# Kernel optimization log

Measured on AMD Instinct MI355X. Metric: run time of the kernel, lower is better.

Reference implementation:

```python
import jax, jax.numpy as jnp
import numpy as np

D_MODEL = 1024
N_HEADS = 16
D_K = 64  # per-head dim and the scaling denominator used by the module
NEG = -1e9  # stand-in for -inf in masked_fill (rows are never fully masked)


def setup_inputs() -> dict:
    key = jax.random.key(0)
    ks = jax.random.split(key, 8)
    B, M, N = 2, 2048, 2048
    q = jax.random.normal(ks[0], (B, M, D_MODEL), dtype=jnp.float32)
    k = jax.random.normal(ks[1], (B, N, D_MODEL), dtype=jnp.float32)
    v = jax.random.normal(ks[2], (B, N, D_MODEL), dtype=jnp.float32)
    mask = jax.random.randint(ks[3], (B, M, N), 0, 2).astype(jnp.bool_)
    # xavier_uniform for square [d,d] weights: limit = sqrt(6/(d+d))
    lim = float(np.sqrt(6.0 / (D_MODEL + D_MODEL)))
    Wq = jax.random.uniform(ks[4], (D_MODEL, D_MODEL), jnp.float32, -lim, lim)
    Wk = jax.random.uniform(ks[5], (D_MODEL, D_MODEL), jnp.float32, -lim, lim)
    Wv = jax.random.uniform(ks[6], (D_MODEL, D_MODEL), jnp.float32, -lim, lim)
    Wo = jax.random.uniform(ks[7], (D_MODEL, D_MODEL), jnp.float32, -lim, lim)
    return {"q": q, "k": k, "v": v, "mask": mask,
            "Wq": Wq, "Wk": Wk, "Wv": Wv, "Wo": Wo}


def _split_heads(x):
    # (B, S, D) -> (B, H, S, Dh); the torch split/cat-on-batch trick is
    # mathematically identical to this standard head reshape.
    B, S, _ = x.shape
    return x.reshape(B, S, N_HEADS, D_K).transpose(0, 2, 1, 3)


def reference(q, k, v, mask, Wq, Wk, Wv, Wo):
    qw = _split_heads(q @ Wq.T)  # (B,H,M,Dh)
    kw = _split_heads(k @ Wk.T)  # (B,H,N,Dh)
    vw = _split_heads(v @ Wv.T)  # (B,H,N,Dh)
    scores = jnp.einsum('bhmd,bhnd->bhmn', qw, kw)
    scores = jnp.where(mask[:, None, :, :], NEG, scores)
    attn = jax.nn.softmax(scores / jnp.sqrt(jnp.float32(D_K)), axis=-1)
    ctx = jnp.einsum('bhmn,bhnd->bhmd', attn, vw)
    B, _, M, _ = ctx.shape
    ctx = ctx.transpose(0, 2, 1, 3).reshape(B, M, D_MODEL)
    return ctx @ Wo.T
```

## Files before the change

kernel.cpp:

```cpp
#include <hip/hip_runtime.h>
#include <hip/hip_bf16.h>
#include <stdint.h>
#include <string.h>

#define SEQ   2048
#define DM    1024
#define NH    16
#define NB    2

typedef __attribute__((ext_vector_type(8))) short bf16x8;
typedef __attribute__((ext_vector_type(4))) float f32x4;
typedef unsigned short u16;
typedef unsigned int   u32;

__device__ __forceinline__ u16 f2bf(float f) {
    u32 u = __float_as_uint(f);
    u += 0x7FFF + ((u >> 16) & 1);
    return (u16)(u >> 16);
}
__device__ __forceinline__ u32 pk2bf(float a, float b) {
    __hip_bfloat162 p = __float22bfloat162_rn(make_float2(a, b));
    u32 u; memcpy(&u, &p, 4); return u;
}
__device__ __forceinline__ float fexp2(float x) {
#if __has_builtin(__builtin_amdgcn_exp2f)
    return __builtin_amdgcn_exp2f(x);
#else
    return exp2f(x);
#endif
}
__device__ __forceinline__ void gl_lds16(const void* g, void* l) {
    __builtin_amdgcn_global_load_lds(
        (const __attribute__((address_space(1))) u32*)g,
        (__attribute__((address_space(3))) u32*)l, 16, 0, 0);
}
__device__ __forceinline__ void wbar_vm3() { asm volatile("s_waitcnt vmcnt(3)\ns_barrier" ::: "memory"); }
__device__ __forceinline__ void wbar_vm4() { asm volatile("s_waitcnt vmcnt(4)\ns_barrier" ::: "memory"); }
__device__ __forceinline__ void wbar_vm6() { asm volatile("s_waitcnt vmcnt(6)\ns_barrier" ::: "memory"); }
__device__ __forceinline__ void vm_drain() { asm volatile("s_waitcnt vmcnt(0)" ::: "memory"); }

struct CvtArgs {
    const float* s[7];
    u16* d[7];
    float scale[7];
    int start[8];
};
__global__ __launch_bounds__(256) void cvt_kernel(CvtArgs a) {
    int bid = blockIdx.x;
    int seg = 0;
#pragma unroll
    for (int i = 1; i < 7; ++i) if (bid >= a.start[i]) seg = i;
    float sc = a.scale[seg];
    size_t base = (size_t)(bid - a.start[seg]) * 2048 + threadIdx.x * 8;
    const float4* s4 = (const float4*)(a.s[seg] + base);
    float4 x = s4[0], y = s4[1];
    u32 r[4];
    r[0] = pk2bf(x.x*sc, x.y*sc); r[1] = pk2bf(x.z*sc, x.w*sc);
    r[2] = pk2bf(y.x*sc, y.y*sc); r[3] = pk2bf(y.z*sc, y.w*sc);
    *(uint4*)(a.d[seg] + base) = *(uint4*)r;
}

__global__ void maskpack_kernel(const int* __restrict__ mask,
                                unsigned int* __restrict__ bits) {
    int gid = blockIdx.x * 256 + threadIdx.x;
    int m = mask[gid];
    unsigned long long bal = __ballot(m != 0);
    int lane = threadIdx.x & 63;
    if (lane == 0)       bits[gid >> 5] = (u32)(bal & 0xFFFFFFFFull);
    else if (lane == 32) bits[gid >> 5] = (u32)(bal >> 32);
}

template<int RT>
__device__ __forceinline__ void gemm_body(const u16* __restrict__ A,
                                          const u16* __restrict__ Bm,
                                          void* __restrict__ Y,
                                          int rtile, int ctile, int mode,
                                          u16* sA, u16* sB) {
    constexpr int ABUF = RT * 32 * 32;
    constexpr int BBUF = 128 * 32;
    const int tid  = threadIdx.x;
    const int wv   = tid >> 6, lane = tid & 63;
    const int quad = lane >> 4, ln = lane & 15;
    const int wr   = wv >> 1,  wc  = wv & 1;

    const int lr4 = lane >> 2;
    const int lcc = ((lane & 3) ^ ((lane >> 3) & 3)) * 8;

    const u16* gA[RT/2]; u16* lA[RT/2];
#pragma unroll
    for (int s = 0; s < RT/2; ++s) {
        int seg = wv * (RT/2) + s;
        gA[s] = A + (size_t)(rtile * (RT*32) + seg*16 + lr4) * 1024 + lcc;
        lA[s] = sA + seg * 512;
    }
    const u16* gB[2]; u16* lB[2];
#pragma unroll
    for (int s = 0; s < 2; ++s) {
        int seg = wv * 2 + s;
        gB[s] = Bm + (size_t)(ctile * 128 + seg*16 + lr4) * 1024 + lcc;
        lB[s] = sB + seg * 512;
    }

    f32x4 acc[RT][4];
#pragma unroll
    for (int i = 0; i < RT; ++i)
#pragma unroll
        for (int j = 0; j < 4; ++j) acc[i][j] = (f32x4){0.f,0.f,0.f,0.f};

    const int c0 = (quad ^ ((ln >> 1) & 3)) * 8;

#pragma unroll
    for (int s = 0; s < RT/2; ++s) gl_lds16(gA[s], lA[s]);
#pragma unroll
    for (int s = 0; s < 2; ++s)    gl_lds16(gB[s], lB[s]);
#pragma unroll
    for (int s = 0; s < RT/2; ++s) gl_lds16(gA[s] + 32, lA[s] + ABUF);
#pragma unroll
    for (int s = 0; s < 2; ++s)    gl_lds16(gB[s] + 32, lB[s] + BBUF);

    int bc = 0, bp = 2;
    for (int kt = 0; kt < 32; ++kt) {
        if (RT == 4) wbar_vm4(); else wbar_vm3();
        int pk = (kt + 2) & 31;
#pragma unroll
        for (int s = 0; s < RT/2; ++s) gl_lds16(gA[s] + pk*32, lA[s] + bp*ABUF);
#pragma unroll
        for (int s = 0; s < 2; ++s)    gl_lds16(gB[s] + pk*32, lB[s] + bp*BBUF);

        const u16* sAb = sA + bc * ABUF;
        const u16* sBb = sB + bc * BBUF;
        bf16x8 af[RT], bfr[4];
#pragma unroll
        for (int rt = 0; rt < RT; ++rt)
            af[rt] = *(const bf16x8*)(sAb + (wr*(RT*16) + rt*16 + ln) * 32 + c0);
#pragma unroll
        for (int ct = 0; ct < 4; ++ct)
            bfr[ct] = *(const bf16x8*)(sBb + (wc*64 + ct*16 + ln) * 32 + c0);
#pragma unroll
        for (int rt = 0; rt < RT; ++rt)
#pragma unroll
            for (int ct = 0; ct < 4; ++ct)
                acc[rt][ct] = __builtin_amdgcn_mfma_f32_16x16x32_bf16(
                    af[rt], bfr[ct], acc[rt][ct], 0, 0, 0);

        bc = (bc == 2) ? 0 : bc + 1;
        bp = (bp == 2) ? 0 : bp + 1;
    }
    vm_drain();

#pragma unroll
    for (int rt = 0; rt < RT; ++rt) {
#pragma unroll
        for (int ct = 0; ct < 4; ++ct) {
#pragma unroll
            for (int i = 0; i < 4; ++i) {
                int R = rtile*(RT*32) + wr*(RT*16) + rt*16 + quad*4 + i;
                int C = ctile*128 + wc*64 + ct*16 + ln;
                float val = acc[rt][ct][i];
                if (mode == 0) {
                    int b = R >> 11, s = R & 2047, h = C >> 6, d = C & 63;
                    ((u16*)Y)[((size_t)((b*NH + h) * SEQ + s) << 6) + d] = f2bf(val);
                } else if (mode == 1) {
                    int h = R >> 6, d = R & 63, b = C >> 11, n = C & 2047;
                    ((u16*)Y)[((size_t)((b*NH + h) * 64 + d) << 11) + n] = f2bf(val);
                } else {
                    ((float*)Y)[(size_t)R * 1024 + C] = val;
                }
            }
        }
    }
}

struct QKVArgs { const u16* A[3]; const u16* B[3]; u16* Y[3]; };

__global__ __launch_bounds__(256) void gemm_qkv(QKVArgs g) {
    __shared__ u16 sA[3 * 128 * 32];
    __shared__ u16 sB[3 * 128 * 32];
    int z = blockIdx.z;
    if (z == 2)
        gemm_body<4>(g.A[2], g.B[2], g.Y[2], blockIdx.y, blockIdx.x, 1, sA, sB);
    else
        gemm_body<4>(g.A[z], g.B[z], g.Y[z], blockIdx.x, blockIdx.y, 0, sA, sB);
}

__global__ __launch_bounds__(256) void gemm_out(const u16* __restrict__ A,
                                                const u16* __restrict__ Bm,
                                                float* __restrict__ Y) {
    __shared__ u16 sA[3 * 64 * 32];
    __shared__ u16 sB[3 * 128 * 32];
    gemm_body<2>(A, Bm, Y, blockIdx.x, blockIdx.y, 2, sA, sB);
}

__global__ __launch_bounds__(256) void attn_kernel(
    const u16* __restrict__ qw,
    const u16* __restrict__ kw,
    const u16* __restrict__ vt,
    const u32* __restrict__ mbits,
    u16* __restrict__ ctx) {

    constexpr int RSD = 36;
    __shared__ u16 sK[3 * 4096];
    __shared__ u16 sV[3 * 4096];
    __shared__ u32 sPd[4 * 32 * RSD];

    const int mtile = blockIdx.x;
    const int bh    = blockIdx.y;
    const int b     = bh >> 4;
    const int tid   = threadIdx.x;
    const int wv    = tid >> 6, lane = tid & 63;
    const int quad  = lane >> 4, ln = lane & 15;
    const int m0    = mtile * 128;

    const size_t hbase = (size_t)bh * SEQ * 64;

    bf16x8 qf[2][2];
#pragma unroll
    for (int mt = 0; mt < 2; ++mt) {
        const u16* qp = qw + hbase + (size_t)(m0 + wv*32 + mt*16 + ln) * 64 + quad*8;
        qf[mt][0] = *(const bf16x8*)(qp);
        qf[mt][1] = *(const bf16x8*)(qp + 32);
    }

    f32x4 o[2][4], lsum[2];
#pragma unroll
    for (int mt = 0; mt < 2; ++mt) {
        lsum[mt] = (f32x4){0.f,0.f,0.f,0.f};
#pragma unroll
        for (int j = 0; j < 4; ++j) o[mt][j] = (f32x4){0.f,0.f,0.f,0.f};
    }

    bf16x8 ones;
#pragma unroll
    for (int i = 0; i < 8; ++i) ones[i] = (short)0x3F80;

    const u32* mrow[2];
#pragma unroll
    for (int mt = 0; mt < 2; ++mt)
        mrow[mt] = mbits + (size_t)(b*SEQ + m0 + wv*32 + mt*16 + ln) * 64;

    const int lr = lane >> 3;
    const int lc = (lane & 7) ^ lr;
    const u16* gK[2]; const u16* gV[2];
    u16 *lK[2], *lV[2];
#pragma unroll
    for (int s = 0; s < 2; ++s) {
        int seg = s * 4 + wv;
        gK[s] = kw + hbase + (size_t)(seg*8 + lr) * 64 + lc*8;
        gV[s] = vt + hbase + (size_t)(seg*8 + lr) * SEQ + lc*8;
        lK[s] = sK + seg * 512;
        lV[s] = sV + seg * 512;
    }

    const int c0 = (quad ^ (ln & 7)) * 8;
    u32* sPw = sPd + wv * 32 * RSD;
    const u16* sP16 = (const u16*)sPd;

#pragma unroll
    for (int s = 0; s < 2; ++s) { gl_lds16(gK[s], lK[s]); gl_lds16(gV[s], lV[s]); }
    uint2 wwA[2], wwB[2], wwC[2];
#pragma unroll
    for (int mt = 0; mt < 2; ++mt) wwA[mt] = *(const uint2*)(mrow[mt]);
#pragma unroll
    for (int s = 0; s < 2; ++s) {
        gl_lds16(gK[s] + 4096, lK[s] + 4096);
        gl_lds16(gV[s] + 64,   lV[s] + 4096);
    }
#pragma unroll
    for (int mt = 0; mt < 2; ++mt) wwB[mt] = *(const uint2*)(mrow[mt] + 2);

    int bc = 0, bp = 2;
    for (int nt = 0; nt < SEQ / 64; ++nt) {
        wbar_vm6();
        int pidx = (nt + 2) & 31;
#pragma unroll
        for (int s = 0; s < 2; ++s) {
            gl_lds16(gK[s] + (size_t)pidx * 4096, lK[s] + bp*4096);
            gl_lds16(gV[s] + pidx * 64,           lV[s] + bp*4096);
        }
#pragma unroll
        for (int mt = 0; mt < 2; ++mt)
            wwC[mt] = *(const uint2*)(mrow[mt] + pidx*2);

        const u16* sKb = sK + bc * 4096;
        const u16* sVb = sV + bc * 4096;

        f32x4 s4[2][4];
#pragma unroll
        for (int ct = 0; ct < 4; ++ct) {
            const u16* kp = sKb + (ct*16 + ln) * 64;
            bf16x8 k0 = *(const bf16x8*)(kp + c0);
            bf16x8 k1 = *(const bf16x8*)(kp + (c0 ^ 32));
#pragma unroll
            for (int mt = 0; mt < 2; ++mt) {
                f32x4 z = (f32x4){0.f, 0.f, 0.f, 0.f};
                z = __builtin_amdgcn_mfma_f32_16x16x32_bf16(k0, qf[mt][0], z, 0, 0, 0);
                z = __builtin_amdgcn_mfma_f32_16x16x32_bf16(k1, qf[mt][1], z, 0, 0, 0);
                s4[mt][ct] = z;
            }
        }

#pragma unroll
        for (int mt = 0; mt < 2; ++mt) {
            u32 w0 = wwA[mt].x >> (quad * 4);
            u32 w1 = wwA[mt].y >> (quad * 4);
#pragma unroll
            for (int ct = 0; ct < 4; ++ct) {
                u32 wsel = (ct & 2) ? w1 : w0;
                float p[4];
#pragma unroll
                for (int i = 0; i < 4; ++i) {
                    bool msk = (wsel >> ((ct & 1) * 16 + i)) & 1u;
                    p[i] = fexp2(msk ? -1e9f : s4[mt][ct][i]);
                }
                uint2 pk;
                pk.x = pk2bf(p[0], p[1]);
                pk.y = pk2bf(p[2], p[3]);
                *(uint2*)(sPw + (mt*16 + ln) * RSD + ct*8 + quad*2) = pk;
            }
        }

#pragma unroll
        for (int mt = 0; mt < 2; ++mt) {
            const u16* pp = sP16 + (wv*32 + mt*16 + ln) * 72;
            bf16x8 pf0 = *(const bf16x8*)(pp + quad*8);
            bf16x8 pf1 = *(const bf16x8*)(pp + 32 + quad*8);
            lsum[mt] = __builtin_amdgcn_mfma_f32_16x16x32_bf16(pf0, ones, lsum[mt], 0, 0, 0);
            lsum[mt] = __builtin_amdgcn_mfma_f32_16x16x32_bf16(pf1, ones, lsum[mt], 0, 0, 0);
#pragma unroll
            for (int ct = 0; ct < 4; ++ct) {
                const u16* vp = sVb + (ct*16 + ln) * 64;
                bf16x8 v0 = *(const bf16x8*)(vp + c0);
                bf16x8 v1 = *(const bf16x8*)(vp + (c0 ^ 32));
                o[mt][ct] = __builtin_amdgcn_mfma_f32_16x16x32_bf16(pf0, v0, o[mt][ct], 0, 0, 0);
                o[mt][ct] = __builtin_amdgcn_mfma_f32_16x16x32_bf16(pf1, v1, o[mt][ct], 0, 0, 0);
            }
        }

        wwA[0] = wwB[0]; wwA[1] = wwB[1];
        wwB[0] = wwC[0]; wwB[1] = wwC[1];
        bc = (bc == 2) ? 0 : bc + 1;
        bp = (bp == 2) ? 0 : bp + 1;
    }
    vm_drain();

#pragma unroll
    for (int mt = 0; mt < 2; ++mt)
#pragma unroll
        for (int i = 0; i < 4; ++i) {
            float inv = 1.f / lsum[mt][i];
            int m = m0 + wv*32 + mt*16 + quad*4 + i;
            size_t base = ((size_t)(b * SEQ + m) << 10) + (bh & 15) * 64;
#pragma unroll
            for (int ct = 0; ct < 4; ++ct)
                ctx[base + ct*16 + ln] = f2bf(o[mt][ct][i] * inv);
        }
}

extern "C" void kernel_launch(void* const* d_in, const int* in_sizes, int n_in,
                              void* d_out, int out_size, void* d_ws, size_t ws_size,
                              hipStream_t stream) {
    const float* q    = (const float*)d_in[0];
    const float* k    = (const float*)d_in[1];
    const float* v    = (const float*)d_in[2];
    const int*   mask = (const int*)d_in[3];
    const float* Wq   = (const float*)d_in[4];
    const float* Wk   = (const float*)d_in[5];
    const float* Wv   = (const float*)d_in[6];
    const float* Wo   = (const float*)d_in[7];
    float* out = (float*)d_out;

    char* ws = (char*)d_ws;
    const size_t SZH = (size_t)NB * SEQ * DM * 2;
    const size_t SZW = (size_t)DM * DM * 2;
    u16* qw   = (u16*)(ws);
    u16* kw   = (u16*)(ws + SZH);
    u16* vt   = (u16*)(ws + 2*SZH);
    u16* ctx  = (u16*)(ws + 3*SZH);
    u16* vb   = ctx;
    u32* mbits= (u32*)(ws + 4*SZH);
    u16* qb   = (u16*)(ws + 4*SZH + (1u<<20));
    u16* kb   = (u16*)(ws + 4*SZH + (1u<<20) + SZH);
    u16* Wqb  = (u16*)(ws + 4*SZH + (1u<<20) + 2*SZH);
    u16* Wkb  = (u16*)((char*)Wqb + SZW);
    u16* Wvb  = (u16*)((char*)Wqb + 2*SZW);
    u16* Wob  = (u16*)((char*)Wqb + 3*SZW);

    const float CSC = 0.18033688011112042f;

    CvtArgs ca;
    ca.s[0]=q;  ca.d[0]=qb;  ca.scale[0]=1.f;
    ca.s[1]=k;  ca.d[1]=kb;  ca.scale[1]=1.f;
    ca.s[2]=v;  ca.d[2]=vb;  ca.scale[2]=1.f;
    ca.s[3]=Wq; ca.d[3]=Wqb; ca.scale[3]=CSC;
    ca.s[4]=Wk; ca.d[4]=Wkb; ca.scale[4]=1.f;
    ca.s[5]=Wv; ca.d[5]=Wvb; ca.scale[5]=1.f;
    ca.s[6]=Wo; ca.d[6]=Wob; ca.scale[6]=1.f;
    int st[8] = {0, 2048, 4096, 6144, 6656, 7168, 7680, 8192};
    for (int i = 0; i < 8; ++i) ca.start[i] = st[i];
    cvt_kernel<<<dim3(8192), dim3(256), 0, stream>>>(ca);

    maskpack_kernel<<<dim3(NB*SEQ*SEQ/256), dim3(256), 0, stream>>>(mask, mbits);

    QKVArgs ga;
    ga.A[0]=qb;  ga.B[0]=Wqb; ga.Y[0]=qw;
    ga.A[1]=kb;  ga.B[1]=Wkb; ga.Y[1]=kw;
    ga.A[2]=Wvb; ga.B[2]=vb;  ga.Y[2]=vt;
    gemm_qkv<<<dim3(32, 8, 3), dim3(256), 0, stream>>>(ga);

    attn_kernel<<<dim3(SEQ/128, NB*NH), dim3(256), 0, stream>>>(qw, kw, vt, mbits, ctx);

    gemm_out<<<dim3(64, 8), dim3(256), 0, stream>>>(ctx, Wob, out);
}
```

Baseline: 276.5 us.

## Split attention block across 8 waves with 16 rows each and bitmask-based masking

The attention kernel now runs 512 threads per block, with each of 8 waves owning 16 query rows instead of 4 waves owning 32. Each wave issues one K and one V async load per tile instead of two, and the wait count changes to match. Masked scores are now zeroed by AND-ing the exp2 result with a sign-extended mask bit, replacing the select-before-exp. This buys more wave-level parallelism and lower register pressure per wave. In exchange, each wave reuses its K/V LDS reads across fewer rows, so LDS read traffic per block goes up.

```diff
diff --git a/kernel.cpp b/kernel.cpp
--- a/kernel.cpp
+++ b/kernel.cpp
@@ -29,6 +29,14 @@
     return exp2f(x);
 #endif
 }
+__device__ __forceinline__ float mask_exp2(float s, u32 lsel, int pos) {
+#if __has_builtin(__builtin_amdgcn_sbfe)
+    u32 keep = (u32)__builtin_amdgcn_sbfe((int)lsel, pos, 1);
+#else
+    u32 keep = (u32)((int)(lsel << (31 - pos)) >> 31);
+#endif
+    return __uint_as_float(__float_as_uint(fexp2(s)) & keep);
+}
 __device__ __forceinline__ void gl_lds16(const void* g, void* l) {
     __builtin_amdgcn_global_load_lds(
         (const __attribute__((address_space(1))) u32*)g,
@@ -36,7 +44,6 @@
 }
 __device__ __forceinline__ void wbar_vm3() { asm volatile("s_waitcnt vmcnt(3)\ns_barrier" ::: "memory"); }
 __device__ __forceinline__ void wbar_vm4() { asm volatile("s_waitcnt vmcnt(4)\ns_barrier" ::: "memory"); }
-__device__ __forceinline__ void wbar_vm6() { asm volatile("s_waitcnt vmcnt(6)\ns_barrier" ::: "memory"); }
 __device__ __forceinline__ void vm_drain() { asm volatile("s_waitcnt vmcnt(0)" ::: "memory"); }
 
 struct CvtArgs {
@@ -191,7 +198,7 @@
     gemm_body<2>(A, Bm, Y, blockIdx.x, blockIdx.y, 2, sA, sB);
 }
 
-__global__ __launch_bounds__(256) void attn_kernel(
+__global__ __launch_bounds__(512) void attn_kernel(
     const u16* __restrict__ qw,
     const u16* __restrict__ kw,
     const u16* __restrict__ vt,
@@ -201,7 +208,7 @@
     constexpr int RSD = 36;
     __shared__ u16 sK[3 * 4096];
     __shared__ u16 sV[3 * 4096];
-    __shared__ u32 sPd[4 * 32 * RSD];
+    __shared__ u32 sPd[8 * 16 * RSD];
 
     const int mtile = blockIdx.x;
     const int bh    = blockIdx.y;
@@ -213,147 +220,114 @@
 
     const size_t hbase = (size_t)bh * SEQ * 64;
 
-    bf16x8 qf[2][2];
-#pragma unroll
-    for (int mt = 0; mt < 2; ++mt) {
-        const u16* qp = qw + hbase + (size_t)(m0 + wv*32 + mt*16 + ln) * 64 + quad*8;
-        qf[mt][0] = *(const bf16x8*)(qp);
-        qf[mt][1] = *(const bf16x8*)(qp + 32);
-    }
-
-    f32x4 o[2][4], lsum[2];
-#pragma unroll
-    for (int mt = 0; mt < 2; ++mt) {
-        lsum[mt] = (f32x4){0.f,0.f,0.f,0.f};
-#pragma unroll
-        for (int j = 0; j < 4; ++j) o[mt][j] = (f32x4){0.f,0.f,0.f,0.f};
-    }
+    bf16x8 qf[2];
+    {
+        const u16* qp = qw + hbase + (size_t)(m0 + wv*16 + ln) * 64 + quad*8;
+        qf[0] = *(const bf16x8*)(qp);
+        qf[1] = *(const bf16x8*)(qp + 32);
+    }
+
+    f32x4 o[4], lsum;
+    lsum = (f32x4){0.f,0.f,0.f,0.f};
+#pragma unroll
+    for (int j = 0; j < 4; ++j) o[j] = (f32x4){0.f,0.f,0.f,0.f};
 
     bf16x8 ones;
 #pragma unroll
     for (int i = 0; i < 8; ++i) ones[i] = (short)0x3F80;
 
-    const u32* mrow[2];
-#pragma unroll
-    for (int mt = 0; mt < 2; ++mt)
-        mrow[mt] = mbits + (size_t)(b*SEQ + m0 + wv*32 + mt*16 + ln) * 64;
+    const u32* mrow = mbits + (size_t)(b*SEQ + m0 + wv*16 + ln) * 64;
 
     const int lr = lane >> 3;
     const int lc = (lane & 7) ^ lr;
-    const u16* gK[2]; const u16* gV[2];
-    u16 *lK[2], *lV[2];
-#pragma unroll
-    for (int s = 0; s < 2; ++s) {
-        int seg = s * 4 + wv;
-        gK[s] = kw + hbase + (size_t)(seg*8 + lr) * 64 + lc*8;
-        gV[s] = vt + hbase + (size_t)(seg*8 + lr) * SEQ + lc*8;
-        lK[s] = sK + seg * 512;
-        lV[s] = sV + seg * 512;
-    }
+    const u16* gK = kw + hbase + (size_t)(wv*8 + lr) * 64 + lc*8;
+    const u16* gV = vt + hbase + (size_t)(wv*8 + lr) * SEQ + lc*8;
+    u16* lK = sK + wv * 512;
+    u16* lV = sV + wv * 512;
 
     const int c0 = (quad ^ (ln & 7)) * 8;
-    u32* sPw = sPd + wv * 32 * RSD;
+    u32* sPw = sPd + wv * 16 * RSD;
     const u16* sP16 = (const u16*)sPd;
 
-#pragma unroll
-    for (int s = 0; s < 2; ++s) { gl_lds16(gK[s], lK[s]); gl_lds16(gV[s], lV[s]); }
-    uint2 wwA[2], wwB[2], wwC[2];
-#pragma unroll
-    for (int mt = 0; mt < 2; ++mt) wwA[mt] = *(const uint2*)(mrow[mt]);
-#pragma unroll
-    for (int s = 0; s < 2; ++s) {
-        gl_lds16(gK[s] + 4096, lK[s] + 4096);
-        gl_lds16(gV[s] + 64,   lV[s] + 4096);
-    }
-#pragma unroll
-    for (int mt = 0; mt < 2; ++mt) wwB[mt] = *(const uint2*)(mrow[mt] + 2);
+    gl_lds16(gK, lK);
+    gl_lds16(gV, lV);
+    uint2 wwA = *(const uint2*)(mrow);
+    gl_lds16(gK + 4096, lK + 4096);
+    gl_lds16(gV + 64,   lV + 4096);
+    uint2 wwB = *(const uint2*)(mrow + 2);
 
     int bc = 0, bp = 2;
     for (int nt = 0; nt < SEQ / 64; ++nt) {
-        wbar_vm6();
+        wbar_vm3();
         int pidx = (nt + 2) & 31;
-#pragma unroll
-        for (int s = 0; s < 2; ++s) {
-            gl_lds16(gK[s] + (size_t)pidx * 4096, lK[s] + bp*4096);
-            gl_lds16(gV[s] + pidx * 64,           lV[s] + bp*4096);
-        }
-#pragma unroll
-        for (int mt = 0; mt < 2; ++mt)
-            wwC[mt] = *(const uint2*)(mrow[mt] + pidx*2);
+        gl_lds16(gK + (size_t)pidx * 4096, lK + bp*4096);
+        gl_lds16(gV + pidx * 64,           lV + bp*4096);
+        uint2 wwC = *(const uint2*)(mrow + pidx*2);
 
         const u16* sKb = sK + bc * 4096;
         const u16* sVb = sV + bc * 4096;
 
-        f32x4 s4[2][4];
+        f32x4 s4[4];
 #pragma unroll
         for (int ct = 0; ct < 4; ++ct) {
             const u16* kp = sKb + (ct*16 + ln) * 64;
             bf16x8 k0 = *(const bf16x8*)(kp + c0);
             bf16x8 k1 = *(const bf16x8*)(kp + (c0 ^ 32));
-#pragma unroll
-            for (int mt = 0; mt < 2; ++mt) {
-                f32x4 z = (f32x4){0.f, 0.f, 0.f, 0.f};
-                z = __builtin_amdgcn_mfma_f32_16x16x32_bf16(k0, qf[mt][0], z, 0, 0, 0);
-                z = __builtin_amdgcn_mfma_f32_16x16x32_bf16(k1, qf[mt][1], z, 0, 0, 0);
-                s4[mt][ct] = z;
-            }
+            f32x4 z = (f32x4){0.f, 0.f, 0.f, 0.f};
+            z = __builtin_amdgcn_mfma_f32_16x16x32_bf16(k0, qf[0], z, 0, 0, 0);
+            z = __builtin_amdgcn_mfma_f32_16x16x32_bf16(k1, qf[1], z, 0, 0, 0);
+            s4[ct] = z;
         }
 
-#pragma unroll
-        for (int mt = 0; mt < 2; ++mt) {
-            u32 w0 = wwA[mt].x >> (quad * 4);
-            u32 w1 = wwA[mt].y >> (quad * 4);
+        {
+            u32 l0 = ~(wwA.x >> (quad * 4));
+            u32 l1 = ~(wwA.y >> (quad * 4));
 #pragma unroll
             for (int ct = 0; ct < 4; ++ct) {
-                u32 wsel = (ct & 2) ? w1 : w0;
+                u32 lsel = (ct & 2) ? l1 : l0;
                 float p[4];
 #pragma unroll
-                for (int i = 0; i < 4; ++i) {
-                    bool msk = (wsel >> ((ct & 1) * 16 + i)) & 1u;
-                    p[i] = fexp2(msk ? -1e9f : s4[mt][ct][i]);
-                }
+                for (int i = 0; i < 4; ++i)
+                    p[i] = mask_exp2(s4[ct][i], lsel, (ct & 1) * 16 + i);
                 uint2 pk;
                 pk.x = pk2bf(p[0], p[1]);
                 pk.y = pk2bf(p[2], p[3]);
-                *(uint2*)(sPw + (mt*16 + ln) * RSD + ct*8 + quad*2) = pk;
+                *(uint2*)(sPw + ln * RSD + ct*8 + quad*2) = pk;
             }
         }
 
-#pragma unroll
-        for (int mt = 0; mt < 2; ++mt) {
-            const u16* pp = sP16 + (wv*32 + mt*16 + ln) * 72;
+        {
+            const u16* pp = sP16 + (wv*16 + ln) * 72;
             bf16x8 pf0 = *(const bf16x8*)(pp + quad*8);
             bf16x8 pf1 = *(const bf16x8*)(pp + 32 + quad*8);
-            lsum[mt] = __builtin_amdgcn_mfma_f32_16x16x32_bf16(pf0, ones, lsum[mt], 0, 0, 0);
-            lsum[mt] = __builtin_amdgcn_mfma_f32_16x16x32_bf16(pf1, ones, lsum[mt], 0, 0, 0);
+            lsum = __builtin_amdgcn_mfma_f32_16x16x32_bf16(pf0, ones, lsum, 0, 0, 0);
+            lsum = __builtin_amdgcn_mfma_f32_16x16x32_bf16(pf1, ones, lsum, 0, 0, 0);
 #pragma unroll
             for (int ct = 0; ct < 4; ++ct) {
                 const u16* vp = sVb + (ct*16 + ln) * 64;
                 bf16x8 v0 = *(const bf16x8*)(vp + c0);
                 bf16x8 v1 = *(const bf16x8*)(vp + (c0 ^ 32));
-                o[mt][ct] = __builtin_amdgcn_mfma_f32_16x16x32_bf16(pf0, v0, o[mt][ct], 0, 0, 0);
-                o[mt][ct] = __builtin_amdgcn_mfma_f32_16x16x32_bf16(pf1, v1, o[mt][ct], 0, 0, 0);
+                o[ct] = __builtin_amdgcn_mfma_f32_16x16x32_bf16(pf0, v0, o[ct], 0, 0, 0);
+                o[ct] = __builtin_amdgcn_mfma_f32_16x16x32_bf16(pf1, v1, o[ct], 0, 0, 0);
             }
         }
 
-        wwA[0] = wwB[0]; wwA[1] = wwB[1];
-        wwB[0] = wwC[0]; wwB[1] = wwC[1];
+        wwA = wwB;
+        wwB = wwC;
         bc = (bc == 2) ? 0 : bc + 1;
         bp = (bp == 2) ? 0 : bp + 1;
     }
     vm_drain();
 
 #pragma unroll
-    for (int mt = 0; mt < 2; ++mt)
-#pragma unroll
-        for (int i = 0; i < 4; ++i) {
-            float inv = 1.f / lsum[mt][i];
-            int m = m0 + wv*32 + mt*16 + quad*4 + i;
-            size_t base = ((size_t)(b * SEQ + m) << 10) + (bh & 15) * 64;
-#pragma unroll
-            for (int ct = 0; ct < 4; ++ct)
-                ctx[base + ct*16 + ln] = f2bf(o[mt][ct][i] * inv);
-        }
+    for (int i = 0; i < 4; ++i) {
+        float inv = 1.f / lsum[i];
+        int m = m0 + wv*16 + quad*4 + i;
+        size_t base = ((size_t)(b * SEQ + m) << 10) + (bh & 15) * 64;
+#pragma unroll
+        for (int ct = 0; ct < 4; ++ct)
+            ctx[base + ct*16 + ln] = f2bf(o[ct][i] * inv);
+    }
 }
 
 extern "C" void kernel_launch(void* const* d_in, const int* in_sizes, int n_in,
@@ -407,7 +381,7 @@
     ga.A[2]=Wvb; ga.B[2]=vb;  ga.Y[2]=vt;
     gemm_qkv<<<dim3(32, 8, 3), dim3(256), 0, stream>>>(ga);
 
-    attn_kernel<<<dim3(SEQ/128, NB*NH), dim3(256), 0, stream>>>(qw, kw, vt, mbits, ctx);
+    attn_kernel<<<dim3(SEQ/128, NB*NH), dim3(512), 0, stream>>>(qw, kw, vt, mbits, ctx);
 
     gemm_out<<<dim3(64, 8), dim3(256), 0, stream>>>(ctx, Wob, out);
 }
```

Result: no change. 274.0 us (-0.9%).

## Split attention key tiles across two wave groups with LDS reduction of partial outputs

Applied to the files above, without the earlier changes.

The attention kernel now launches 512 threads per block. Two groups of four waves each process half of every 64-key tile for the same 128 query rows. The partial outputs and row sums are combined through shared memory at the end. Masking is now a bitfield-extract AND on the exp2 result instead of a select. The aim is more waves per block to hide latency, at the cost of a larger LDS footprint, extra barriers and a final reduction pass.

```diff
diff --git a/kernel.cpp b/kernel.cpp
--- a/kernel.cpp
+++ b/kernel.cpp
@@ -29,6 +29,14 @@
     return exp2f(x);
 #endif
 }
+__device__ __forceinline__ float mask_exp2(float s, u32 lsel, int pos) {
+#if __has_builtin(__builtin_amdgcn_sbfe)
+    u32 keep = (u32)__builtin_amdgcn_sbfe((int)lsel, pos, 1);
+#else
+    u32 keep = (u32)((int)(lsel << (31 - pos)) >> 31);
+#endif
+    return __uint_as_float(__float_as_uint(fexp2(s)) & keep);
+}
 __device__ __forceinline__ void gl_lds16(const void* g, void* l) {
     __builtin_amdgcn_global_load_lds(
         (const __attribute__((address_space(1))) u32*)g,
@@ -36,7 +44,6 @@
 }
 __device__ __forceinline__ void wbar_vm3() { asm volatile("s_waitcnt vmcnt(3)\ns_barrier" ::: "memory"); }
 __device__ __forceinline__ void wbar_vm4() { asm volatile("s_waitcnt vmcnt(4)\ns_barrier" ::: "memory"); }
-__device__ __forceinline__ void wbar_vm6() { asm volatile("s_waitcnt vmcnt(6)\ns_barrier" ::: "memory"); }
 __device__ __forceinline__ void vm_drain() { asm volatile("s_waitcnt vmcnt(0)" ::: "memory"); }
 
 struct CvtArgs {
@@ -191,17 +198,18 @@
     gemm_body<2>(A, Bm, Y, blockIdx.x, blockIdx.y, 2, sA, sB);
 }
 
-__global__ __launch_bounds__(256) void attn_kernel(
+__global__ __launch_bounds__(512, 4) void attn_kernel(
     const u16* __restrict__ qw,
     const u16* __restrict__ kw,
     const u16* __restrict__ vt,
     const u32* __restrict__ mbits,
     u16* __restrict__ ctx) {
 
-    constexpr int RSD = 36;
-    __shared__ u16 sK[3 * 4096];
-    __shared__ u16 sV[3 * 4096];
-    __shared__ u32 sPd[4 * 32 * RSD];
+    constexpr int RSD = 18;
+    __shared__ __align__(16) char smem[67584];
+    u16* sK  = (u16*)smem;
+    u16* sV  = (u16*)(smem + 24576);
+    u32* sPd = (u32*)(smem + 49152);
 
     const int mtile = blockIdx.x;
     const int bh    = blockIdx.y;
@@ -209,6 +217,8 @@
     const int tid   = threadIdx.x;
     const int wv    = tid >> 6, lane = tid & 63;
     const int quad  = lane >> 4, ln = lane & 15;
+    const int g     = wv >> 2;
+    const int w2    = wv & 3;
     const int m0    = mtile * 128;
 
     const size_t hbase = (size_t)bh * SEQ * 64;
@@ -216,7 +226,7 @@
     bf16x8 qf[2][2];
 #pragma unroll
     for (int mt = 0; mt < 2; ++mt) {
-        const u16* qp = qw + hbase + (size_t)(m0 + wv*32 + mt*16 + ln) * 64 + quad*8;
+        const u16* qp = qw + hbase + (size_t)(m0 + w2*32 + mt*16 + ln) * 64 + quad*8;
         qf[mt][0] = *(const bf16x8*)(qp);
         qf[mt][1] = *(const bf16x8*)(qp + 32);
     }
@@ -236,58 +246,45 @@
     const u32* mrow[2];
 #pragma unroll
     for (int mt = 0; mt < 2; ++mt)
-        mrow[mt] = mbits + (size_t)(b*SEQ + m0 + wv*32 + mt*16 + ln) * 64;
+        mrow[mt] = mbits + (size_t)(b*SEQ + m0 + w2*32 + mt*16 + ln) * 64 + g;
 
     const int lr = lane >> 3;
     const int lc = (lane & 7) ^ lr;
-    const u16* gK[2]; const u16* gV[2];
-    u16 *lK[2], *lV[2];
-#pragma unroll
-    for (int s = 0; s < 2; ++s) {
-        int seg = s * 4 + wv;
-        gK[s] = kw + hbase + (size_t)(seg*8 + lr) * 64 + lc*8;
-        gV[s] = vt + hbase + (size_t)(seg*8 + lr) * SEQ + lc*8;
-        lK[s] = sK + seg * 512;
-        lV[s] = sV + seg * 512;
-    }
-
-    const int c0 = (quad ^ (ln & 7)) * 8;
+    const u16* gK = kw + hbase + (size_t)(wv*8 + lr) * 64 + lc*8;
+    const u16* gV = vt + hbase + (size_t)(wv*8 + lr) * SEQ + lc*8;
+    u16* lK = sK + wv * 512;
+    u16* lV = sV + wv * 512;
+
+    const int c0  = (quad ^ (ln & 7)) * 8;
+    const int c0v = (((g*4 + quad) ^ (ln & 7))) * 8;
     u32* sPw = sPd + wv * 32 * RSD;
-    const u16* sP16 = (const u16*)sPd;
-
-#pragma unroll
-    for (int s = 0; s < 2; ++s) { gl_lds16(gK[s], lK[s]); gl_lds16(gV[s], lV[s]); }
-    uint2 wwA[2], wwB[2], wwC[2];
-#pragma unroll
-    for (int mt = 0; mt < 2; ++mt) wwA[mt] = *(const uint2*)(mrow[mt]);
-#pragma unroll
-    for (int s = 0; s < 2; ++s) {
-        gl_lds16(gK[s] + 4096, lK[s] + 4096);
-        gl_lds16(gV[s] + 64,   lV[s] + 4096);
-    }
-#pragma unroll
-    for (int mt = 0; mt < 2; ++mt) wwB[mt] = *(const uint2*)(mrow[mt] + 2);
+
+    gl_lds16(gK, lK);
+    gl_lds16(gV, lV);
+    u32 wwA[2], wwB[2], wwC[2];
+#pragma unroll
+    for (int mt = 0; mt < 2; ++mt) wwA[mt] = mrow[mt][0];
+    gl_lds16(gK + 4096, lK + 4096);
+    gl_lds16(gV + 64,   lV + 4096);
+#pragma unroll
+    for (int mt = 0; mt < 2; ++mt) wwB[mt] = mrow[mt][2];
 
     int bc = 0, bp = 2;
     for (int nt = 0; nt < SEQ / 64; ++nt) {
-        wbar_vm6();
+        wbar_vm4();
         int pidx = (nt + 2) & 31;
-#pragma unroll
-        for (int s = 0; s < 2; ++s) {
-            gl_lds16(gK[s] + (size_t)pidx * 4096, lK[s] + bp*4096);
-            gl_lds16(gV[s] + pidx * 64,           lV[s] + bp*4096);
-        }
-#pragma unroll
-        for (int mt = 0; mt < 2; ++mt)
-            wwC[mt] = *(const uint2*)(mrow[mt] + pidx*2);
+        gl_lds16(gK + (size_t)pidx * 4096, lK + bp*4096);
+        gl_lds16(gV + pidx * 64,           lV + bp*4096);
+#pragma unroll
+        for (int mt = 0; mt < 2; ++mt) wwC[mt] = mrow[mt][pidx*2];
 
         const u16* sKb = sK + bc * 4096;
         const u16* sVb = sV + bc * 4096;
 
-        f32x4 s4[2][4];
-#pragma unroll
-        for (int ct = 0; ct < 4; ++ct) {
-            const u16* kp = sKb + (ct*16 + ln) * 64;
+        f32x4 s4[2][2];
+#pragma unroll
+        for (int ct2 = 0; ct2 < 2; ++ct2) {
+            const u16* kp = sKb + (g*32 + ct2*16 + ln) * 64;
             bf16x8 k0 = *(const bf16x8*)(kp + c0);
             bf16x8 k1 = *(const bf16x8*)(kp + (c0 ^ 32));
 #pragma unroll
@@ -295,44 +292,35 @@
                 f32x4 z = (f32x4){0.f, 0.f, 0.f, 0.f};
                 z = __builtin_amdgcn_mfma_f32_16x16x32_bf16(k0, qf[mt][0], z, 0, 0, 0);
                 z = __builtin_amdgcn_mfma_f32_16x16x32_bf16(k1, qf[mt][1], z, 0, 0, 0);
-                s4[mt][ct] = z;
+                s4[mt][ct2] = z;
             }
         }
 
 #pragma unroll
         for (int mt = 0; mt < 2; ++mt) {
-            u32 w0 = wwA[mt].x >> (quad * 4);
-            u32 w1 = wwA[mt].y >> (quad * 4);
-#pragma unroll
-            for (int ct = 0; ct < 4; ++ct) {
-                u32 wsel = (ct & 2) ? w1 : w0;
+            u32 l = ~(wwA[mt] >> (quad * 4));
+#pragma unroll
+            for (int ct2 = 0; ct2 < 2; ++ct2) {
                 float p[4];
 #pragma unroll
-                for (int i = 0; i < 4; ++i) {
-                    bool msk = (wsel >> ((ct & 1) * 16 + i)) & 1u;
-                    p[i] = fexp2(msk ? -1e9f : s4[mt][ct][i]);
-                }
+                for (int i = 0; i < 4; ++i)
+                    p[i] = mask_exp2(s4[mt][ct2][i], l, ct2 * 16 + i);
                 uint2 pk;
                 pk.x = pk2bf(p[0], p[1]);
                 pk.y = pk2bf(p[2], p[3]);
-                *(uint2*)(sPw + (mt*16 + ln) * RSD + ct*8 + quad*2) = pk;
+                *(uint2*)(sPw + (mt*16 + ln) * RSD + ct2*8 + quad*2) = pk;
             }
         }
 
 #pragma unroll
         for (int mt = 0; mt < 2; ++mt) {
-            const u16* pp = sP16 + (wv*32 + mt*16 + ln) * 72;
-            bf16x8 pf0 = *(const bf16x8*)(pp + quad*8);
-            bf16x8 pf1 = *(const bf16x8*)(pp + 32 + quad*8);
-            lsum[mt] = __builtin_amdgcn_mfma_f32_16x16x32_bf16(pf0, ones, lsum[mt], 0, 0, 0);
-            lsum[mt] = __builtin_amdgcn_mfma_f32_16x16x32_bf16(pf1, ones, lsum[mt], 0, 0, 0);
+            uint4 praw = *(const uint4*)(sPw + (mt*16 + ln) * RSD + quad*4);
+            bf16x8 pf; memcpy(&pf, &praw, 16);
+            lsum[mt] = __builtin_amdgcn_mfma_f32_16x16x32_bf16(pf, ones, lsum[mt], 0, 0, 0);
 #pragma unroll
             for (int ct = 0; ct < 4; ++ct) {
-                const u16* vp = sVb + (ct*16 + ln) * 64;
-                bf16x8 v0 = *(const bf16x8*)(vp + c0);
-                bf16x8 v1 = *(const bf16x8*)(vp + (c0 ^ 32));
-                o[mt][ct] = __builtin_amdgcn_mfma_f32_16x16x32_bf16(pf0, v0, o[mt][ct], 0, 0, 0);
-                o[mt][ct] = __builtin_amdgcn_mfma_f32_16x16x32_bf16(pf1, v1, o[mt][ct], 0, 0, 0);
+                bf16x8 vf = *(const bf16x8*)(sVb + (ct*16 + ln) * 64 + c0v);
+                o[mt][ct] = __builtin_amdgcn_mfma_f32_16x16x32_bf16(pf, vf, o[mt][ct], 0, 0, 0);
             }
         }
 
@@ -342,18 +330,38 @@
         bp = (bp == 2) ? 0 : bp + 1;
     }
     vm_drain();
-
-#pragma unroll
-    for (int mt = 0; mt < 2; ++mt)
-#pragma unroll
-        for (int i = 0; i < 4; ++i) {
-            float inv = 1.f / lsum[mt][i];
-            int m = m0 + wv*32 + mt*16 + quad*4 + i;
-            size_t base = ((size_t)(b * SEQ + m) << 10) + (bh & 15) * 64;
-#pragma unroll
-            for (int ct = 0; ct < 4; ++ct)
-                ctx[base + ct*16 + ln] = f2bf(o[mt][ct][i] * inv);
-        }
+    __syncthreads();
+
+    float* sO  = (float*)smem;
+    float* sLs = (float*)(smem + 33280);
+    if (g == 1) {
+#pragma unroll
+        for (int mt = 0; mt < 2; ++mt)
+#pragma unroll
+            for (int i = 0; i < 4; ++i) {
+                int lm = w2*32 + mt*16 + quad*4 + i;
+                sLs[lm] = lsum[mt][i];
+#pragma unroll
+                for (int ct = 0; ct < 4; ++ct)
+                    sO[lm*65 + ct*16 + ln] = o[mt][ct][i];
+            }
+    }
+    __syncthreads();
+    if (g == 0) {
+#pragma unroll
+        for (int mt = 0; mt < 2; ++mt)
+#pragma unroll
+            for (int i = 0; i < 4; ++i) {
+                int lm = w2*32 + mt*16 + quad*4 + i;
+                float inv = 1.f / (lsum[mt][i] + sLs[lm]);
+                int m = m0 + lm;
+                size_t base = ((size_t)(b * SEQ + m) << 10) + (bh & 15) * 64;
+#pragma unroll
+                for (int ct = 0; ct < 4; ++ct)
+                    ctx[base + ct*16 + ln] =
+                        f2bf((o[mt][ct][i] + sO[lm*65 + ct*16 + ln]) * inv);
+            }
+    }
 }
 
 extern "C" void kernel_launch(void* const* d_in, const int* in_sizes, int n_in,
@@ -407,7 +415,7 @@
     ga.A[2]=Wvb; ga.B[2]=vb;  ga.Y[2]=vt;
     gemm_qkv<<<dim3(32, 8, 3), dim3(256), 0, stream>>>(ga);
 
-    attn_kernel<<<dim3(SEQ/128, NB*NH), dim3(256), 0, stream>>>(qw, kw, vt, mbits, ctx);
+    attn_kernel<<<dim3(SEQ/128, NB*NH), dim3(512), 0, stream>>>(qw, kw, vt, mbits, ctx);
 
     gemm_out<<<dim3(64, 8), dim3(256), 0, stream>>>(ctx, Wob, out);
 }
```

New measurement: 277.0 us. No clear change (+0.2%).
